# Kernel tuning notes

Hardware: AMD Instinct MI355X
Metric: run time of the kernel (lower is better)

The kernel has to match this reference:

```python
import jax, jax.numpy as jnp
import numpy as np


def _glorot(key, shape):
    lim = np.sqrt(6.0 / (shape[-2] + shape[-1])).astype(np.float32)
    return jax.random.uniform(key, shape, jnp.float32, -lim, lim)


def setup_inputs() -> dict:
    key = jax.random.key(0)
    B, F, K, L = 8192, 256, 32768, 4
    H = 2 * F          # CouplingLayer(feat_size, feat_size * 2) hidden width
    half = F // 2      # affine coupling transforms half the features
    ks = jax.random.split(key, 6)
    return {
        "inputs": jax.random.normal(ks[0], (B, F), jnp.float32),
        "W1": _glorot(ks[1], (L, half, H)),
        "b1": jnp.zeros((L, H), jnp.float32),
        "Ws": _glorot(ks[2], (L, H, half)),
        "bs": jnp.zeros((L, half), jnp.float32),
        "Wt": _glorot(ks[3], (L, H, half)),
        "bt": jnp.zeros((L, half), jnp.float32),
        "prior": _glorot(ks[4], (K, F)),  # VQ codebook, GlorotUniform init as in source
    }


def _forward_flow(x, W1, b1, Ws, bs, Wt, bt):
    """Stack of affine coupling layers; returns (y, log|det J|) per sample."""
    L = W1.shape[0]
    jac = jnp.zeros((x.shape[0],), x.dtype)
    for l in range(L):  # small fixed layer count
        xa, xb = jnp.split(x, 2, axis=1)                 # [B, F/2] each
        h = jax.nn.relu(xa @ W1[l] + b1[l])              # [B, 2F]
        s_raw = h @ Ws[l] + bs[l]                        # [B, F/2]
        s = s_raw if l == L - 1 else jnp.tanh(s_raw)     # last layer: tf.identity
        t = h @ Wt[l] + bt[l]
        yb = xb * jnp.exp(s) + t
        jac = jac + jnp.sum(s, axis=1)
        x = jnp.concatenate([yb, xa], axis=1)            # swap halves for mixing
    return x, jac


def reference(inputs, W1, b1, Ws, bs, Wt, bt, prior):
    sg = jax.lax.stop_gradient
    x, jac = _forward_flow(inputs, W1, b1, Ws, bs, Wt, bt)   # [B, F], [B]
    # pairwise squared distance to codebook: [B, K]
    na = jnp.sum(x * x, axis=1, keepdims=True)               # [B, 1]
    nb = jnp.sum(prior * prior, axis=1)[None, :]             # [1, K]
    d = jnp.maximum(na - 2.0 * (x @ prior.T) + nb, 0.0)      # [B, K]
    target_ind = jnp.argmin(d, axis=1)                       # [B]
    target = prior[target_ind]                               # gather, [B, F]
    loss_1 = jnp.mean(jnp.sum((x - sg(target)) ** 2, axis=1) / 2)
    loss_2 = jnp.mean(jnp.sum((sg(x) - target) ** 2, axis=1) / 2)
    loss = loss_1 + 0.25 * loss_2 - jnp.mean(jac)
    return x, loss
```

## Files before the change

### kernel.cpp

```cpp
#include <hip/hip_runtime.h>
#include <hip/hip_fp8.h>
#include <stdint.h>

#define NB     8192
#define NF     256
#define NHALF  128
#define NHID   512
#define NLAY   4
#define NK     32768

#define SX     (1.0f / 16.0f)
#define SP     (256.0f)

typedef __attribute__((ext_vector_type(8))) short bf16x8;
typedef __attribute__((ext_vector_type(4))) float f32x4;
typedef __attribute__((ext_vector_type(8))) int i32x8;

static __device__ __forceinline__ unsigned short f2bf(float f) {
  union { float f; unsigned int u; } v; v.f = f;
  return (unsigned short)((v.u + 0x7FFFu + ((v.u >> 16) & 1u)) >> 16);
}
static __device__ __forceinline__ float bf2f(unsigned short u) {
  union { unsigned int u; float f; } v; v.u = ((unsigned int)u) << 16; return v.f;
}
static __device__ __forceinline__ unsigned char f2fp8(float f) {
  __hip_fp8_e4m3 q(f);
  return (unsigned char)q.__x;
}
static __device__ __forceinline__ float fp82f(unsigned char b) {
  __hip_fp8_e4m3 q; q.__x = b; return (float)q;
}

static __device__ __forceinline__ void load_lds16(const void* g, void* l) {
  __builtin_amdgcn_global_load_lds(
      (const __attribute__((address_space(1))) unsigned int*)g,
      (__attribute__((address_space(3))) unsigned int*)l, 16, 0, 0);
}

static __device__ __forceinline__ unsigned long long packsi(float v, int idx) {
  unsigned int b = __float_as_uint(v);
  b = (b & 0x80000000u) ? ~b : (b | 0x80000000u);
  return ((unsigned long long)b << 32) | (unsigned int)(~(unsigned int)idx);
}

static __device__ __forceinline__ float fast_tanh(float x) {
  const float xc = fminf(fmaxf(x, -15.f), 15.f);
  const float e2 = __expf(2.f * xc);
  return 1.f - 2.f / (e2 + 1.f);
}

static __device__ __forceinline__ int swadr(int kseg, int nrows, int row, int kin) {
  return (kseg * nrows + row) * 64 + (((kin >> 3) ^ (row & 7)) * 8) + (kin & 7);
}

static __device__ __forceinline__ int g1swz(int row) {
  return (row & 15) ^ ((row & 8) >> 1);
}

static __device__ __forceinline__ void stage_chunk(
    int g, unsigned short* dst,
    const unsigned short* __restrict__ W1T,
    const unsigned short* __restrict__ W2I,
    int wave, int lane, int bxr)
{
  const int l = g >> 3;
  const int nc = ((g & 7) + bxr) & 7;
  const unsigned short* W1l = W1T + (size_t)l * (NHID * NHALF) + (size_t)nc * 64 * 128;
#pragma unroll
  for (int u = 0; u < 2; u++) {
    const int ch = (u * 8 + wave) * 64 + lane;
    const int row = ch >> 4, sl = ch & 15;
    load_lds16(W1l + (size_t)row * 128 + (sl ^ g1swz(row)) * 8, dst + ch * 8);
  }
  const unsigned short* W2l = W2I + (size_t)l * (NF * NHID) + nc * 64;
#pragma unroll
  for (int u = 0; u < 4; u++) {
    const int ch = (u * 8 + wave) * 64 + lane;
    const int col = ch >> 3, sl = ch & 7;
    load_lds16(W2l + (size_t)col * NHID + ((sl ^ (col & 7)) * 8),
               dst + 8192 + ch * 8);
  }
}

__global__ __launch_bounds__(512, 2)
void flow_all(const float* __restrict__ in,
              const unsigned short* __restrict__ W1T,
              const unsigned short* __restrict__ W2I,
              const float* __restrict__ b1A,
              const float* __restrict__ bsA,
              const float* __restrict__ btA,
              float* __restrict__ xout,
              unsigned char* __restrict__ xf8,
              float* __restrict__ jac)
{
  __shared__ __align__(16) unsigned short Xb[2][32 * 128];
  __shared__ __align__(16) unsigned short Bs[2][24576];
  __shared__ float b1s[NLAY * NHID];
  __shared__ float bss[NLAY * NHALF];
  __shared__ float bts[NLAY * NHALF];
  __shared__ float jlds[4][32];
  const int tid = threadIdx.x;
  const int lane = tid & 63, wave = tid >> 6;
  const int rg = wave >> 2, cg = wave & 3;
  const int q = lane >> 4, c = lane & 15;
  const int m0 = blockIdx.x * 32;
  const int bxr = blockIdx.x & 7;

  stage_chunk(0, Bs[0], W1T, W2I, wave, lane, bxr);

#pragma unroll
  for (int v = 0; v < 4; v++) {
    const int t4 = tid + v * 512;
    const int row = t4 >> 6, f4 = t4 & 63;
    const float4 d = *(const float4*)(in + (size_t)(m0 + row) * NF + f4 * 4);
    unsigned short* dst = Xb[f4 >> 5];
    const int feat = (f4 & 31) * 4;
    const float vals[4] = {d.x, d.y, d.z, d.w};
#pragma unroll
    for (int u = 0; u < 4; u++) {
      const int fe = feat + u;
      dst[swadr(fe >> 6, 32, row, fe & 63)] = f2bf(vals[u]);
    }
  }

#pragma unroll
  for (int v = 0; v < 4; v++) b1s[tid + v * 512] = b1A[tid + v * 512];
  bss[tid] = bsA[tid];
  bts[tid] = btA[tid];

  stage_chunk(1, Bs[1], W1T, W2I, wave, lane, bxr);

  float jr[4] = {0.f, 0.f, 0.f, 0.f};
  bf16x8 af1[4];
  const f32x4 z = {0.f, 0.f, 0.f, 0.f};
  f32x4 acc2[4];

  for (int g = 0; g < 32; g++) {
    if (g < 31)
      asm volatile("s_waitcnt vmcnt(6) lgkmcnt(0)\n\ts_barrier" ::: "memory");
    else
      asm volatile("s_waitcnt vmcnt(0) lgkmcnt(0)\n\ts_barrier" ::: "memory");

    const int l = g >> 3, s = g & 7;
    const int nc = (s + bxr) & 7;
    const unsigned short* B = Bs[g & 1];
    const unsigned short* W2B = B + 8192;
    unsigned short* XA = Xb[l & 1];
    unsigned short* XB = Xb[1 - (l & 1)];

    if (s == 0) {
#pragma unroll
      for (int kw = 0; kw < 4; kw++) {
        const int kch = kw * 4 + q;
        af1[kw] = *(const bf16x8*)(XA + ((kch >> 3) * 32 + rg * 16 + c) * 64 +
                                   (((kch & 7) ^ (c & 7)) * 8));
      }
#pragma unroll
      for (int j = 0; j < 4; j++) acc2[j] = z;
    }

    const int bias_base = l * NHID + nc * 64;
#pragma unroll
    for (int P = 0; P < 2; P++) {
      union { unsigned int u[4]; bf16x8 v; } a2;
#pragma unroll
      for (int tb = 0; tb < 2; tb++) {
        f32x4 acc1 = z;
        const int row = P * 32 + 8 * (c >> 2) + (c & 3) + 4 * tb;
        const int gsw = g1swz(row);
#pragma unroll
        for (int kk = 0; kk < 4; kk++) {
          const bf16x8 a1 = *(const bf16x8*)(B + row * 128 +
                                             (((kk * 4 + q) ^ gsw) * 8));
          acc1 = __builtin_amdgcn_mfma_f32_16x16x32_bf16(a1, af1[kk], acc1, 0, 0, 0);
        }
        const float4 bb = *(const float4*)(b1s + bias_base + P * 32 + 8 * q + 4 * tb);
        const float v0 = fmaxf(acc1[0] + bb.x, 0.f);
        const float v1 = fmaxf(acc1[1] + bb.y, 0.f);
        const float v2 = fmaxf(acc1[2] + bb.z, 0.f);
        const float v3 = fmaxf(acc1[3] + bb.w, 0.f);
        a2.u[tb * 2]     = (unsigned int)f2bf(v0) | ((unsigned int)f2bf(v1) << 16);
        a2.u[tb * 2 + 1] = (unsigned int)f2bf(v2) | ((unsigned int)f2bf(v3) << 16);
      }
#pragma unroll
      for (int j = 0; j < 4; j++) {
        const int col = cg * 64 + 16 * j + c;
        const bf16x8 b2 = *(const bf16x8*)(W2B + col * 64 +
                                           (((P * 4 + q) ^ (col & 7)) * 8));
        acc2[j] = __builtin_amdgcn_mfma_f32_16x16x32_bf16(a2.v, b2, acc2[j], 0, 0, 0);
      }
    }

    if (s == 7) {
      const int parity = c & 1;
      const int lastl = (l == NLAY - 1);
      const float* bsl = bss + l * NHALF;
      const float* btl = bts + l * NHALF;
#pragma unroll
      for (int j = 0; j < 4; j++) {
        const int col = cg * 64 + 16 * j + c;
#pragma unroll
        for (int r = 0; r < 4; r++) {
          const float val = acc2[j][r];
          const float oth = __shfl_xor(val, 1);
          if (!parity) {
            const int feat = col >> 1;
            float sv = val + bsl[feat];
            if (!lastl) sv = fast_tanh(sv);
            const float t = oth + btl[feat];
            const int row = rg * 16 + 4 * q + r;
            const int xaddr = swadr(feat >> 6, 32, row, feat & 63);
            const float xb = bf2f(XB[xaddr]);
            const float yb = xb * __expf(sv) + t;
            jr[r] += sv;
            XB[xaddr] = f2bf(yb);
            if (l >= 2) {
              const int k = lastl ? feat : (NHALF + feat);
              const size_t grow = (size_t)(m0 + row) * NF;
              xout[grow + k] = yb;
              xf8[(size_t)(m0 + row) * 256 + k] = f2fp8(yb * SX);
            }
          }
        }
      }
    }

    asm volatile("s_waitcnt lgkmcnt(0)\n\ts_barrier" ::: "memory");
    if (g + 2 < 32) stage_chunk(g + 2, Bs[g & 1], W1T, W2I, wave, lane, bxr);
  }

#pragma unroll
  for (int r = 0; r < 4; r++) {
    float v = jr[r];
    v += __shfl_xor(v, 1); v += __shfl_xor(v, 2);
    v += __shfl_xor(v, 4); v += __shfl_xor(v, 8);
    if (c == 0) jlds[cg][rg * 16 + 4 * q + r] = v;
  }
  __syncthreads();
  if (tid < 32)
    jac[m0 + tid] = jlds[0][tid] + jlds[1][tid] + jlds[2][tid] + jlds[3][tid];
}

__global__ __launch_bounds__(256, 2)
void vq_argmax(const unsigned char* __restrict__ X8,
               const unsigned char* __restrict__ P8,
               const float* __restrict__ nbh,
               unsigned long long* __restrict__ gbest)
{
  __shared__ __align__(16) unsigned char Bs[2][64 * 256];
  const int tid = threadIdx.x;
  const int lane = tid & 63, wave = tid >> 6;
  const int y = blockIdx.x & 15;
  const int m0 = (blockIdx.x >> 4) * 256;
  const int q = lane >> 4, c = lane & 15;
  const int mw = m0 + wave * 64;
  const int one = 0x7F7F7F7F;

  i32x8 af[4][2];
#pragma unroll
  for (int i = 0; i < 4; i++) {
    const unsigned char* xr = X8 + (size_t)(mw + 16 * i + c) * 256 + q * 32;
#pragma unroll
    for (int h = 0; h < 2; h++) {
      const int4 lo = *(const int4*)(xr + h * 128);
      const int4 hi = *(const int4*)(xr + h * 128 + 16);
      af[i][h] = (i32x8){lo.x, lo.y, lo.z, lo.w, hi.x, hi.y, hi.z, hi.w};
    }
  }

  float bestv[16];
  int besti[16];
#pragma unroll
  for (int t = 0; t < 16; t++) { bestv[t] = -1e30f; besti[t] = 0; }

  {
    const int n0s = y * 2048;
#pragma unroll
    for (int u = 0; u < 4; u++) {
      const int chb = (u * 4 + wave) * 64;
      const int ch = chb + lane;
      const int row = ch >> 4, gslot = ch & 15;
      load_lds16(P8 + (size_t)(n0s + row) * 256 + (gslot ^ (row & 15)) * 16,
                 Bs[0] + chb * 16);
    }
  }

  for (int nt = 0; nt < 32; nt++) {
    const int n0 = y * 2048 + nt * 64;
    __syncthreads();

    float nbr[4];
#pragma unroll
    for (int j = 0; j < 4; j++) nbr[j] = nbh[n0 + 16 * j + c];

    if (nt + 1 < 32) {
      const int n0s = n0 + 64;
      unsigned char* dst = Bs[(nt + 1) & 1];
#pragma unroll
      for (int u = 0; u < 4; u++) {
        const int chb = (u * 4 + wave) * 64;
        const int ch = chb + lane;
        const int row = ch >> 4, gslot = ch & 15;
        load_lds16(P8 + (size_t)(n0s + row) * 256 + (gslot ^ (row & 15)) * 16,
                   dst + chb * 16);
      }
    }

    const unsigned char* Bt = Bs[nt & 1];
    f32x4 acc[4][4];
#pragma unroll
    for (int i = 0; i < 4; i++)
#pragma unroll
      for (int j = 0; j < 4; j++)
        acc[i][j] = (f32x4){-nbr[j], -nbr[j], -nbr[j], -nbr[j]};

#pragma unroll
    for (int j = 0; j < 4; j++) {
      const unsigned char* base = Bt + (16 * j + c) * 256;
#pragma unroll
      for (int h = 0; h < 2; h++) {
        const int4 b0 = *(const int4*)(base + ((8 * h + 2 * q)     ^ c) * 16);
        const int4 b1 = *(const int4*)(base + ((8 * h + 2 * q + 1) ^ c) * 16);
        const i32x8 bf = (i32x8){b0.x, b0.y, b0.z, b0.w, b1.x, b1.y, b1.z, b1.w};
#pragma unroll
        for (int i = 0; i < 4; i++)
          acc[i][j] = __builtin_amdgcn_mfma_scale_f32_16x16x128_f8f6f4(
              af[i][h], bf, acc[i][j], 0, 0, 0, one, 0, one);
      }
    }

#pragma unroll
    for (int j = 0; j < 4; j++) {
      const int col = n0 + 16 * j + c;
#pragma unroll
      for (int i = 0; i < 4; i++)
#pragma unroll
        for (int r = 0; r < 4; r++) {
          const float sc = acc[i][j][r];
          const int t = i * 4 + r;
          if (sc > bestv[t]) { bestv[t] = sc; besti[t] = col; }
        }
    }
  }

#pragma unroll
  for (int t = 0; t < 16; t++) {
    float lv = bestv[t]; int li = besti[t];
#pragma unroll
    for (int mk = 8; mk >= 1; mk >>= 1) {
      const float ov = __shfl_xor(lv, mk);
      const int oi = __shfl_xor(li, mk);
      if (ov > lv || (ov == lv && oi < li)) { lv = ov; li = oi; }
    }
    if (c == 0) {
      const int row = mw + 16 * (t >> 2) + q * 4 + (t & 3);
      atomicMax(&gbest[row], packsi(lv, li));
    }
  }
}

__global__ void prep_all(const float* __restrict__ W1,
                         const float* __restrict__ Ws,
                         const float* __restrict__ Wt,
                         const float* __restrict__ prior,
                         unsigned short* __restrict__ W1T,
                         unsigned short* __restrict__ W2I,
                         unsigned char* __restrict__ p8,
                         float* __restrict__ nbh,
                         unsigned long long* __restrict__ gbest,
                         float* __restrict__ accum)
{
  __shared__ float ts[64 * 65];
  const int bx = blockIdx.x;
  const int tid = threadIdx.x;
  if (bx < 2048) {
    const int k = bx * 16 + (tid >> 4);
    const int l16 = tid & 15;
    float s = 0.f;
#pragma unroll
    for (int v = 0; v < 4; v++) {
      const int off = (v * 16 + l16) * 4;
      const float4 d = *(const float4*)(prior + (size_t)k * NF + off);
      uchar4 o;
      o.x = f2fp8(d.x * SP); o.y = f2fp8(d.y * SP);
      o.z = f2fp8(d.z * SP); o.w = f2fp8(d.w * SP);
      *(uchar4*)(p8 + (size_t)k * 256 + off) = o;
      const float q0 = fp82f(o.x), q1 = fp82f(o.y), q2 = fp82f(o.z), q3 = fp82f(o.w);
      s += q0 * q0 + q1 * q1 + q2 * q2 + q3 * q3;
    }
#pragma unroll
    for (int mk = 8; mk >= 1; mk >>= 1) s += __shfl_xor(s, mk);
    if (l16 == 0) nbh[k] = 0.5f * s * (SX / SP);
  } else if (bx < 2112) {
    const int job = bx - 2048;
    const int l = job >> 4, t = job & 15;
    const int k0 = (t >> 3) * 64, n0 = (t & 7) * 64;
    const float* src = W1 + (size_t)l * NHALF * NHID;
#pragma unroll
    for (int v = 0; v < 16; v++) {
      const int e = tid + v * 256;
      const int kk = e >> 6, nn = e & 63;
      ts[kk * 65 + nn] = src[(size_t)(k0 + kk) * NHID + n0 + nn];
    }
    __syncthreads();
    unsigned short* dst = W1T + (size_t)l * NHID * NHALF;
#pragma unroll
    for (int v = 0; v < 16; v++) {
      const int e = tid + v * 256;
      const int nn = e >> 6, kk = e & 63;
      dst[(size_t)(n0 + nn) * NHALF + k0 + kk] = f2bf(ts[kk * 65 + nn]);
    }
  } else if (bx < 2240) {
    const int job = bx - 2112;
    const int l = job >> 5, rem = job & 31;
    const int b = rem >> 4;
    const int k0 = ((rem >> 1) & 7) * 64;
    const int f0 = (rem & 1) * 64;
    const float* src = (b ? Wt : Ws) + (size_t)l * NHID * NHALF;
#pragma unroll
    for (int v = 0; v < 16; v++) {
      const int e = tid + v * 256;
      const int kk = e >> 6, nn = e & 63;
      ts[kk * 65 + nn] = src[(size_t)(k0 + kk) * NHALF + f0 + nn];
    }
    __syncthreads();
#pragma unroll
    for (int v = 0; v < 16; v++) {
      const int e = tid + v * 256;
      const int nn = e >> 6, kk = e & 63;
      W2I[((size_t)l * NF + 2 * (f0 + nn) + b) * NHID + k0 + kk] = f2bf(ts[kk * 65 + nn]);
    }
  } else {
    const int idx = (bx - 2240) * 256 + tid;
    if (idx < NB) gbest[idx] = 0ull;
    if (idx < 4) accum[idx] = 0.f;
  }
}

__global__ void vq_finalize(const float* __restrict__ X,
                            const float* __restrict__ prior,
                            const unsigned long long* __restrict__ gbest,
                            const float* __restrict__ jac,
                            float* __restrict__ accum,
                            float* __restrict__ loss)
{
  const int wave = threadIdx.x >> 6, lane = threadIdx.x & 63;
  const int gw = blockIdx.x * 4 + wave;
  float accd = 0.f, accj = 0.f;
  for (int r = 0; r < 8; r++) {
    const int row = gw * 8 + r;
    const unsigned int idx = ~(unsigned int)(gbest[row]);
    const float* x = X + (size_t)row * NF;
    const float* p = prior + (size_t)idx * NF;
#pragma unroll
    for (int u = 0; u < 4; u++) {
      const int d = lane + u * 64;
      const float df = x[d] - p[d];
      accd += df * df;
    }
    if (lane == 0) accj += jac[row];
  }
#pragma unroll
  for (int mk = 32; mk >= 1; mk >>= 1) {
    accd += __shfl_xor(accd, mk);
    accj += __shfl_xor(accj, mk);
  }
  __shared__ float sd[4], sj[4];
  if (lane == 0) { sd[wave] = accd; sj[wave] = accj; }
  __syncthreads();
  if (threadIdx.x == 0) {
    atomicAdd(&accum[0], sd[0] + sd[1] + sd[2] + sd[3]);
    atomicAdd(&accum[1], sj[0] + sj[1] + sj[2] + sj[3]);
    __threadfence();
    const unsigned int t = atomicAdd((unsigned int*)&accum[2], 1u);
    if (t == 255u) {
      const float d = atomicAdd(&accum[0], 0.f);
      const float jv = atomicAdd(&accum[1], 0.f);
      loss[0] = 1.25f * (0.5f * d / (float)NB) - jv / (float)NB;
    }
  }
}

extern "C" void kernel_launch(void* const* d_in, const int* in_sizes, int n_in,
                              void* d_out, int out_size, void* d_ws, size_t ws_size,
                              hipStream_t stream)
{
  (void)in_sizes; (void)n_in; (void)out_size; (void)ws_size;
  const float* inputs = (const float*)d_in[0];
  const float* W1 = (const float*)d_in[1];
  const float* b1 = (const float*)d_in[2];
  const float* Ws = (const float*)d_in[3];
  const float* bs = (const float*)d_in[4];
  const float* Wt = (const float*)d_in[5];
  const float* bt = (const float*)d_in[6];
  const float* prior = (const float*)d_in[7];

  char* p = (char*)d_ws;
  auto alloc = [&](size_t bytes) { char* r = p; p += (bytes + 255) & ~(size_t)255; return r; };
  unsigned short* W1T  = (unsigned short*)alloc((size_t)NLAY * NHID * NHALF * 2);
  unsigned short* W2I  = (unsigned short*)alloc((size_t)NLAY * NF * NHID * 2);
  unsigned char* P8    = (unsigned char*)alloc((size_t)NK * 256);
  float* NBH           = (float*)alloc((size_t)NK * 4);
  unsigned char* XF8   = (unsigned char*)alloc((size_t)NB * 256);
  float* JAC           = (float*)alloc((size_t)NB * 4);
  unsigned long long* GBEST = (unsigned long long*)alloc((size_t)NB * 8);
  float* ACC           = (float*)alloc(256);

  float* xout = (float*)d_out;
  float* loss = xout + (size_t)NB * NF;

  prep_all<<<dim3(2272), 256, 0, stream>>>(
      W1, Ws, Wt, prior, W1T, W2I, P8, NBH, GBEST, ACC);

  flow_all<<<dim3(NB / 32), 512, 0, stream>>>(
      inputs, W1T, W2I, b1, bs, bt, xout, XF8, JAC);

  vq_argmax<<<dim3(32 * 16), 256, 0, stream>>>(XF8, P8, NBH, GBEST);
  vq_finalize<<<dim3(256), 256, 0, stream>>>(xout, prior, GBEST, JAC, ACC, loss);
}
```

Baseline: 237.4 us.

## Fuse codebook fp8 quantization into flow kernel and finalize into argmax kernel

Measured after the change: 305.4 us. 28.6% more time.

```diff
diff --git a/kernel.cpp b/kernel.cpp
--- a/kernel.cpp
+++ b/kernel.cpp
@@ -16,6 +16,15 @@
 typedef __attribute__((ext_vector_type(4))) float f32x4;
 typedef __attribute__((ext_vector_type(8))) int i32x8;
 
+#if defined(__has_builtin)
+#  if __has_builtin(__builtin_amdgcn_cvt_pk_fp8_f32)
+#    define HAVE_HW_FP8_ENC 1
+#  endif
+#  if __has_builtin(__builtin_amdgcn_cvt_f32_fp8)
+#    define HAVE_HW_FP8_DEC 1
+#  endif
+#endif
+
 static __device__ __forceinline__ unsigned short f2bf(float f) {
   union { float f; unsigned int u; } v; v.f = f;
   return (unsigned short)((v.u + 0x7FFFu + ((v.u >> 16) & 1u)) >> 16);
@@ -23,12 +32,34 @@
 static __device__ __forceinline__ float bf2f(unsigned short u) {
   union { unsigned int u; float f; } v; v.u = ((unsigned int)u) << 16; return v.f;
 }
-static __device__ __forceinline__ unsigned char f2fp8(float f) {
+static __device__ __forceinline__ unsigned char f2fp8_sw(float f) {
   __hip_fp8_e4m3 q(f);
   return (unsigned char)q.__x;
 }
-static __device__ __forceinline__ float fp82f(unsigned char b) {
-  __hip_fp8_e4m3 q; q.__x = b; return (float)q;
+static __device__ __forceinline__ unsigned char f2fp8(float f) {
+#ifdef HAVE_HW_FP8_ENC
+  return (unsigned char)(__builtin_amdgcn_cvt_pk_fp8_f32(f, f, 0, false) & 0xff);
+#else
+  return f2fp8_sw(f);
+#endif
+}
+static __device__ __forceinline__ unsigned int fp8x4(float a, float b, float c, float d) {
+#ifdef HAVE_HW_FP8_ENC
+  int v = __builtin_amdgcn_cvt_pk_fp8_f32(a, b, 0, false);
+  v = __builtin_amdgcn_cvt_pk_fp8_f32(c, d, v, true);
+  return (unsigned int)v;
+#else
+  return (unsigned int)f2fp8_sw(a) | ((unsigned int)f2fp8_sw(b) << 8) |
+         ((unsigned int)f2fp8_sw(c) << 16) | ((unsigned int)f2fp8_sw(d) << 24);
+#endif
+}
+template <int SEL>
+static __device__ __forceinline__ float fp8dec(unsigned int w) {
+#ifdef HAVE_HW_FP8_DEC
+  return __builtin_amdgcn_cvt_f32_fp8((int)w, SEL);
+#else
+  __hip_fp8_e4m3 q; q.__x = (unsigned char)(w >> (8 * SEL)); return (float)q;
+#endif
 }
 
 static __device__ __forceinline__ void load_lds16(const void* g, void* l) {
@@ -82,15 +113,18 @@
   }
 }
 
-__global__ __launch_bounds__(512, 2)
+__global__ __launch_bounds__(768, 1)
 void flow_all(const float* __restrict__ in,
               const unsigned short* __restrict__ W1T,
               const unsigned short* __restrict__ W2I,
               const float* __restrict__ b1A,
               const float* __restrict__ bsA,
               const float* __restrict__ btA,
+              const float* __restrict__ prior,
               float* __restrict__ xout,
               unsigned char* __restrict__ xf8,
+              unsigned char* __restrict__ p8,
+              float* __restrict__ nbh,
               float* __restrict__ jac)
 {
   __shared__ __align__(16) unsigned short Xb[2][32 * 128];
@@ -101,34 +135,35 @@
   __shared__ float jlds[4][32];
   const int tid = threadIdx.x;
   const int lane = tid & 63, wave = tid >> 6;
-  const int rg = wave >> 2, cg = wave & 3;
+  const int rg = (wave >> 2) & 1, cg = wave & 3;
   const int q = lane >> 4, c = lane & 15;
   const int m0 = blockIdx.x * 32;
   const int bxr = blockIdx.x & 7;
 
-  stage_chunk(0, Bs[0], W1T, W2I, wave, lane, bxr);
-
-#pragma unroll
-  for (int v = 0; v < 4; v++) {
-    const int t4 = tid + v * 512;
-    const int row = t4 >> 6, f4 = t4 & 63;
-    const float4 d = *(const float4*)(in + (size_t)(m0 + row) * NF + f4 * 4);
-    unsigned short* dst = Xb[f4 >> 5];
-    const int feat = (f4 & 31) * 4;
-    const float vals[4] = {d.x, d.y, d.z, d.w};
-#pragma unroll
-    for (int u = 0; u < 4; u++) {
-      const int fe = feat + u;
-      dst[swadr(fe >> 6, 32, row, fe & 63)] = f2bf(vals[u]);
-    }
-  }
-
-#pragma unroll
-  for (int v = 0; v < 4; v++) b1s[tid + v * 512] = b1A[tid + v * 512];
-  bss[tid] = bsA[tid];
-  bts[tid] = btA[tid];
-
-  stage_chunk(1, Bs[1], W1T, W2I, wave, lane, bxr);
+  if (wave < 8) stage_chunk(0, Bs[0], W1T, W2I, wave, lane, bxr);
+
+  if (tid < 512) {
+#pragma unroll
+    for (int v = 0; v < 4; v++) {
+      const int t4 = tid + v * 512;
+      const int row = t4 >> 6, f4 = t4 & 63;
+      const float4 d = *(const float4*)(in + (size_t)(m0 + row) * NF + f4 * 4);
+      unsigned short* dst = Xb[f4 >> 5];
+      const int feat = (f4 & 31) * 4;
+      const float vals[4] = {d.x, d.y, d.z, d.w};
+#pragma unroll
+      for (int u = 0; u < 4; u++) {
+        const int fe = feat + u;
+        dst[swadr(fe >> 6, 32, row, fe & 63)] = f2bf(vals[u]);
+      }
+    }
+#pragma unroll
+    for (int v = 0; v < 4; v++) b1s[tid + v * 512] = b1A[tid + v * 512];
+    bss[tid] = bsA[tid];
+    bts[tid] = btA[tid];
+  }
+
+  if (wave < 8) stage_chunk(1, Bs[1], W1T, W2I, wave, lane, bxr);
 
   float jr[4] = {0.f, 0.f, 0.f, 0.f};
   bf16x8 af1[4];
@@ -136,105 +171,122 @@
   f32x4 acc2[4];
 
   for (int g = 0; g < 32; g++) {
-    if (g < 31)
-      asm volatile("s_waitcnt vmcnt(6) lgkmcnt(0)\n\ts_barrier" ::: "memory");
-    else
-      asm volatile("s_waitcnt vmcnt(0) lgkmcnt(0)\n\ts_barrier" ::: "memory");
-
-    const int l = g >> 3, s = g & 7;
-    const int nc = (s + bxr) & 7;
-    const unsigned short* B = Bs[g & 1];
-    const unsigned short* W2B = B + 8192;
-    unsigned short* XA = Xb[l & 1];
-    unsigned short* XB = Xb[1 - (l & 1)];
-
-    if (s == 0) {
-#pragma unroll
-      for (int kw = 0; kw < 4; kw++) {
-        const int kch = kw * 4 + q;
-        af1[kw] = *(const bf16x8*)(XA + ((kch >> 3) * 32 + rg * 16 + c) * 64 +
-                                   (((kch & 7) ^ (c & 7)) * 8));
-      }
-#pragma unroll
-      for (int j = 0; j < 4; j++) acc2[j] = z;
-    }
-
-    const int bias_base = l * NHID + nc * 64;
-#pragma unroll
-    for (int P = 0; P < 2; P++) {
-      union { unsigned int u[4]; bf16x8 v; } a2;
-#pragma unroll
-      for (int tb = 0; tb < 2; tb++) {
-        f32x4 acc1 = z;
-        const int row = P * 32 + 8 * (c >> 2) + (c & 3) + 4 * tb;
-        const int gsw = g1swz(row);
-#pragma unroll
-        for (int kk = 0; kk < 4; kk++) {
-          const bf16x8 a1 = *(const bf16x8*)(B + row * 128 +
-                                             (((kk * 4 + q) ^ gsw) * 8));
-          acc1 = __builtin_amdgcn_mfma_f32_16x16x32_bf16(a1, af1[kk], acc1, 0, 0, 0);
+    if (wave < 8) {
+      if (g < 31)
+        asm volatile("s_waitcnt vmcnt(6) lgkmcnt(0)\n\ts_barrier" ::: "memory");
+      else
+        asm volatile("s_waitcnt vmcnt(0) lgkmcnt(0)\n\ts_barrier" ::: "memory");
+
+      const int l = g >> 3, s = g & 7;
+      const int nc = (s + bxr) & 7;
+      const unsigned short* B = Bs[g & 1];
+      const unsigned short* W2B = B + 8192;
+      unsigned short* XA = Xb[l & 1];
+      unsigned short* XB = Xb[1 - (l & 1)];
+
+      if (s == 0) {
+#pragma unroll
+        for (int kw = 0; kw < 4; kw++) {
+          const int kch = kw * 4 + q;
+          af1[kw] = *(const bf16x8*)(XA + ((kch >> 3) * 32 + rg * 16 + c) * 64 +
+                                     (((kch & 7) ^ (c & 7)) * 8));
         }
-        const float4 bb = *(const float4*)(b1s + bias_base + P * 32 + 8 * q + 4 * tb);
-        const float v0 = fmaxf(acc1[0] + bb.x, 0.f);
-        const float v1 = fmaxf(acc1[1] + bb.y, 0.f);
-        const float v2 = fmaxf(acc1[2] + bb.z, 0.f);
-        const float v3 = fmaxf(acc1[3] + bb.w, 0.f);
-        a2.u[tb * 2]     = (unsigned int)f2bf(v0) | ((unsigned int)f2bf(v1) << 16);
-        a2.u[tb * 2 + 1] = (unsigned int)f2bf(v2) | ((unsigned int)f2bf(v3) << 16);
-      }
-#pragma unroll
-      for (int j = 0; j < 4; j++) {
-        const int col = cg * 64 + 16 * j + c;
-        const bf16x8 b2 = *(const bf16x8*)(W2B + col * 64 +
-                                           (((P * 4 + q) ^ (col & 7)) * 8));
-        acc2[j] = __builtin_amdgcn_mfma_f32_16x16x32_bf16(a2.v, b2, acc2[j], 0, 0, 0);
-      }
-    }
-
-    if (s == 7) {
-      const int parity = c & 1;
-      const int lastl = (l == NLAY - 1);
-      const float* bsl = bss + l * NHALF;
-      const float* btl = bts + l * NHALF;
-#pragma unroll
-      for (int j = 0; j < 4; j++) {
-        const int col = cg * 64 + 16 * j + c;
-#pragma unroll
-        for (int r = 0; r < 4; r++) {
-          const float val = acc2[j][r];
-          const float oth = __shfl_xor(val, 1);
-          if (!parity) {
-            const int feat = col >> 1;
-            float sv = val + bsl[feat];
-            if (!lastl) sv = fast_tanh(sv);
-            const float t = oth + btl[feat];
-            const int row = rg * 16 + 4 * q + r;
-            const int xaddr = swadr(feat >> 6, 32, row, feat & 63);
-            const float xb = bf2f(XB[xaddr]);
-            const float yb = xb * __expf(sv) + t;
-            jr[r] += sv;
-            XB[xaddr] = f2bf(yb);
-            if (l >= 2) {
-              const int k = lastl ? feat : (NHALF + feat);
-              const size_t grow = (size_t)(m0 + row) * NF;
-              xout[grow + k] = yb;
-              xf8[(size_t)(m0 + row) * 256 + k] = f2fp8(yb * SX);
+#pragma unroll
+        for (int j = 0; j < 4; j++) acc2[j] = z;
+      }
+
+      const int bias_base = l * NHID + nc * 64;
+#pragma unroll
+      for (int P = 0; P < 2; P++) {
+        union { unsigned int u[4]; bf16x8 v; } a2;
+#pragma unroll
+        for (int tb = 0; tb < 2; tb++) {
+          f32x4 acc1 = z;
+          const int row = P * 32 + 8 * (c >> 2) + (c & 3) + 4 * tb;
+          const int gsw = g1swz(row);
+#pragma unroll
+          for (int kk = 0; kk < 4; kk++) {
+            const bf16x8 a1 = *(const bf16x8*)(B + row * 128 +
+                                               (((kk * 4 + q) ^ gsw) * 8));
+            acc1 = __builtin_amdgcn_mfma_f32_16x16x32_bf16(a1, af1[kk], acc1, 0, 0, 0);
+          }
+          const float4 bb = *(const float4*)(b1s + bias_base + P * 32 + 8 * q + 4 * tb);
+          const float v0 = fmaxf(acc1[0] + bb.x, 0.f);
+          const float v1 = fmaxf(acc1[1] + bb.y, 0.f);
+          const float v2 = fmaxf(acc1[2] + bb.z, 0.f);
+          const float v3 = fmaxf(acc1[3] + bb.w, 0.f);
+          a2.u[tb * 2]     = (unsigned int)f2bf(v0) | ((unsigned int)f2bf(v1) << 16);
+          a2.u[tb * 2 + 1] = (unsigned int)f2bf(v2) | ((unsigned int)f2bf(v3) << 16);
+        }
+#pragma unroll
+        for (int j = 0; j < 4; j++) {
+          const int col = cg * 64 + 16 * j + c;
+          const bf16x8 b2 = *(const bf16x8*)(W2B + col * 64 +
+                                             (((P * 4 + q) ^ (col & 7)) * 8));
+          acc2[j] = __builtin_amdgcn_mfma_f32_16x16x32_bf16(a2.v, b2, acc2[j], 0, 0, 0);
+        }
+      }
+
+      if (s == 7) {
+        const int parity = c & 1;
+        const int lastl = (l == NLAY - 1);
+        const float* bsl = bss + l * NHALF;
+        const float* btl = bts + l * NHALF;
+#pragma unroll
+        for (int j = 0; j < 4; j++) {
+          const int col = cg * 64 + 16 * j + c;
+#pragma unroll
+          for (int r = 0; r < 4; r++) {
+            const float val = acc2[j][r];
+            const float oth = __shfl_xor(val, 1);
+            if (!parity) {
+              const int feat = col >> 1;
+              float sv = val + bsl[feat];
+              if (!lastl) sv = fast_tanh(sv);
+              const float t = oth + btl[feat];
+              const int row = rg * 16 + 4 * q + r;
+              const int xaddr = swadr(feat >> 6, 32, row, feat & 63);
+              const float xb = bf2f(XB[xaddr]);
+              const float yb = xb * __expf(sv) + t;
+              jr[r] += sv;
+              XB[xaddr] = f2bf(yb);
+              if (l >= 2) {
+                const int k = lastl ? feat : (NHALF + feat);
+                const size_t grow = (size_t)(m0 + row) * NF;
+                xout[grow + k] = yb;
+                xf8[(size_t)(m0 + row) * 256 + k] = f2fp8(yb * SX);
+              }
             }
           }
         }
       }
-    }
-
-    asm volatile("s_waitcnt lgkmcnt(0)\n\ts_barrier" ::: "memory");
-    if (g + 2 < 32) stage_chunk(g + 2, Bs[g & 1], W1T, W2I, wave, lane, bxr);
-  }
-
-#pragma unroll
-  for (int r = 0; r < 4; r++) {
-    float v = jr[r];
-    v += __shfl_xor(v, 1); v += __shfl_xor(v, 2);
-    v += __shfl_xor(v, 4); v += __shfl_xor(v, 8);
-    if (c == 0) jlds[cg][rg * 16 + 4 * q + r] = v;
+
+      asm volatile("s_waitcnt lgkmcnt(0)\n\ts_barrier" ::: "memory");
+      if (g + 2 < 32) stage_chunk(g + 2, Bs[g & 1], W1T, W2I, wave, lane, bxr);
+    } else {
+      const int code = (((int)blockIdx.x * 4 + (wave - 8)) << 5) + g;
+      const float4 d = *(const float4*)(prior + (size_t)code * NF + lane * 4);
+      const unsigned int w4 = fp8x4(d.x * SP, d.y * SP, d.z * SP, d.w * SP);
+      *(unsigned int*)(p8 + (size_t)code * 256 + lane * 4) = w4;
+      const float q0 = fp8dec<0>(w4), q1 = fp8dec<1>(w4);
+      const float q2 = fp8dec<2>(w4), q3 = fp8dec<3>(w4);
+      float s = q0 * q0 + q1 * q1 + q2 * q2 + q3 * q3;
+#pragma unroll
+      for (int mk = 32; mk >= 1; mk >>= 1) s += __shfl_xor(s, mk);
+      if (lane == 0) nbh[code] = 0.5f * s * (SX / SP);
+      asm volatile("s_barrier" ::: "memory");
+      asm volatile("s_barrier" ::: "memory");
+    }
+  }
+
+  if (wave < 8) {
+#pragma unroll
+    for (int r = 0; r < 4; r++) {
+      float v = jr[r];
+      v += __shfl_xor(v, 1); v += __shfl_xor(v, 2);
+      v += __shfl_xor(v, 4); v += __shfl_xor(v, 8);
+      if (c == 0) jlds[cg][rg * 16 + 4 * q + r] = v;
+    }
   }
   __syncthreads();
   if (tid < 32)
@@ -245,13 +297,20 @@
 void vq_argmax(const unsigned char* __restrict__ X8,
                const unsigned char* __restrict__ P8,
                const float* __restrict__ nbh,
-               unsigned long long* __restrict__ gbest)
+               unsigned long long* __restrict__ gbest,
+               const float* __restrict__ X,
+               const float* __restrict__ priorF,
+               const float* __restrict__ jac,
+               float* __restrict__ accum,
+               unsigned int* __restrict__ tick,
+               float* __restrict__ loss)
 {
   __shared__ __align__(16) unsigned char Bs[2][64 * 256];
   const int tid = threadIdx.x;
   const int lane = tid & 63, wave = tid >> 6;
   const int y = blockIdx.x & 15;
-  const int m0 = (blockIdx.x >> 4) * 256;
+  const int mgrp = blockIdx.x >> 4;
+  const int m0 = mgrp * 256;
   const int q = lane >> 4, c = lane & 15;
   const int mw = m0 + wave * 64;
   const int one = 0x7F7F7F7F;
@@ -357,42 +416,65 @@
       atomicMax(&gbest[row], packsi(lv, li));
     }
   }
-}
-
-__global__ void prep_all(const float* __restrict__ W1,
-                         const float* __restrict__ Ws,
-                         const float* __restrict__ Wt,
-                         const float* __restrict__ prior,
-                         unsigned short* __restrict__ W1T,
-                         unsigned short* __restrict__ W2I,
-                         unsigned char* __restrict__ p8,
-                         float* __restrict__ nbh,
-                         unsigned long long* __restrict__ gbest,
-                         float* __restrict__ accum)
+
+  __threadfence();
+  __shared__ int lastf;
+  if (tid == 0) lastf = (atomicAdd(&tick[mgrp], 1u) == 15u);
+  __syncthreads();
+  if (lastf) {
+    __threadfence();
+    float accd = 0.f, accj = 0.f;
+    for (int r = 0; r < 64; r++) {
+      const int row = m0 + wave * 64 + r;
+      unsigned long long gv = 0ull;
+      if (lane == 0) gv = atomicMax(&gbest[row], 0ull);
+      gv = __shfl(gv, 0);
+      const unsigned int idx = ~(unsigned int)gv;
+      const float* xr = X + (size_t)row * NF;
+      const float* pr = priorF + (size_t)idx * NF;
+#pragma unroll
+      for (int u = 0; u < 4; u++) {
+        const int dd = lane + u * 64;
+        const float df = xr[dd] - pr[dd];
+        accd += df * df;
+      }
+      if (lane == 0) accj += jac[row];
+    }
+#pragma unroll
+    for (int mk = 32; mk >= 1; mk >>= 1) {
+      accd += __shfl_xor(accd, mk);
+      accj += __shfl_xor(accj, mk);
+    }
+    __shared__ float sd[4], sj[4];
+    if (lane == 0) { sd[wave] = accd; sj[wave] = accj; }
+    __syncthreads();
+    if (tid == 0) {
+      atomicAdd(&accum[0], sd[0] + sd[1] + sd[2] + sd[3]);
+      atomicAdd(&accum[1], sj[0] + sj[1] + sj[2] + sj[3]);
+      __threadfence();
+      const unsigned int t2 = atomicAdd((unsigned int*)&accum[2], 1u);
+      if (t2 == 31u) {
+        const float dsum = atomicAdd(&accum[0], 0.f);
+        const float jsum = atomicAdd(&accum[1], 0.f);
+        loss[0] = 1.25f * (0.5f * dsum / (float)NB) - jsum / (float)NB;
+      }
+    }
+  }
+}
+
+__global__ void prep_W(const float* __restrict__ W1,
+                       const float* __restrict__ Ws,
+                       const float* __restrict__ Wt,
+                       unsigned short* __restrict__ W1T,
+                       unsigned short* __restrict__ W2I,
+                       unsigned long long* __restrict__ gbest,
+                       float* __restrict__ accum)
 {
   __shared__ float ts[64 * 65];
   const int bx = blockIdx.x;
   const int tid = threadIdx.x;
-  if (bx < 2048) {
-    const int k = bx * 16 + (tid >> 4);
-    const int l16 = tid & 15;
-    float s = 0.f;
-#pragma unroll
-    for (int v = 0; v < 4; v++) {
-      const int off = (v * 16 + l16) * 4;
-      const float4 d = *(const float4*)(prior + (size_t)k * NF + off);
-      uchar4 o;
-      o.x = f2fp8(d.x * SP); o.y = f2fp8(d.y * SP);
-      o.z = f2fp8(d.z * SP); o.w = f2fp8(d.w * SP);
-      *(uchar4*)(p8 + (size_t)k * 256 + off) = o;
-      const float q0 = fp82f(o.x), q1 = fp82f(o.y), q2 = fp82f(o.z), q3 = fp82f(o.w);
-      s += q0 * q0 + q1 * q1 + q2 * q2 + q3 * q3;
-    }
-#pragma unroll
-    for (int mk = 8; mk >= 1; mk >>= 1) s += __shfl_xor(s, mk);
-    if (l16 == 0) nbh[k] = 0.5f * s * (SX / SP);
-  } else if (bx < 2112) {
-    const int job = bx - 2048;
+  if (bx < 64) {
+    const int job = bx;
     const int l = job >> 4, t = job & 15;
     const int k0 = (t >> 3) * 64, n0 = (t & 7) * 64;
     const float* src = W1 + (size_t)l * NHALF * NHID;
@@ -410,8 +492,8 @@
       const int nn = e >> 6, kk = e & 63;
       dst[(size_t)(n0 + nn) * NHALF + k0 + kk] = f2bf(ts[kk * 65 + nn]);
     }
-  } else if (bx < 2240) {
-    const int job = bx - 2112;
+  } else if (bx < 192) {
+    const int job = bx - 64;
     const int l = job >> 5, rem = job & 31;
     const int b = rem >> 4;
     const int k0 = ((rem >> 1) & 7) * 64;
@@ -431,53 +513,9 @@
       W2I[((size_t)l * NF + 2 * (f0 + nn) + b) * NHID + k0 + kk] = f2bf(ts[kk * 65 + nn]);
     }
   } else {
-    const int idx = (bx - 2240) * 256 + tid;
+    const int idx = (bx - 192) * 256 + tid;
     if (idx < NB) gbest[idx] = 0ull;
-    if (idx < 4) accum[idx] = 0.f;
-  }
-}
-
-__global__ void vq_finalize(const float* __restrict__ X,
-                            const float* __restrict__ prior,
-                            const unsigned long long* __restrict__ gbest,
-                            const float* __restrict__ jac,
-                            float* __restrict__ accum,
-                            float* __restrict__ loss)
-{
-  const int wave = threadIdx.x >> 6, lane = threadIdx.x & 63;
-  const int gw = blockIdx.x * 4 + wave;
-  float accd = 0.f, accj = 0.f;
-  for (int r = 0; r < 8; r++) {
-    const int row = gw * 8 + r;
-    const unsigned int idx = ~(unsigned int)(gbest[row]);
-    const float* x = X + (size_t)row * NF;
-    const float* p = prior + (size_t)idx * NF;
-#pragma unroll
-    for (int u = 0; u < 4; u++) {
-      const int d = lane + u * 64;
-      const float df = x[d] - p[d];
-      accd += df * df;
-    }
-    if (lane == 0) accj += jac[row];
-  }
-#pragma unroll
-  for (int mk = 32; mk >= 1; mk >>= 1) {
-    accd += __shfl_xor(accd, mk);
-    accj += __shfl_xor(accj, mk);
-  }
-  __shared__ float sd[4], sj[4];
-  if (lane == 0) { sd[wave] = accd; sj[wave] = accj; }
-  __syncthreads();
-  if (threadIdx.x == 0) {
-    atomicAdd(&accum[0], sd[0] + sd[1] + sd[2] + sd[3]);
-    atomicAdd(&accum[1], sj[0] + sj[1] + sj[2] + sj[3]);
-    __threadfence();
-    const unsigned int t = atomicAdd((unsigned int*)&accum[2], 1u);
-    if (t == 255u) {
-      const float d = atomicAdd(&accum[0], 0.f);
-      const float jv = atomicAdd(&accum[1], 0.f);
-      loss[0] = 1.25f * (0.5f * d / (float)NB) - jv / (float)NB;
-    }
+    if (idx < 64) accum[idx] = 0.f;
   }
 }
 
@@ -505,16 +543,16 @@
   float* JAC           = (float*)alloc((size_t)NB * 4);
   unsigned long long* GBEST = (unsigned long long*)alloc((size_t)NB * 8);
   float* ACC           = (float*)alloc(256);
+  unsigned int* TICK   = (unsigned int*)(ACC + 8);
 
   float* xout = (float*)d_out;
   float* loss = xout + (size_t)NB * NF;
 
-  prep_all<<<dim3(2272), 256, 0, stream>>>(
-      W1, Ws, Wt, prior, W1T, W2I, P8, NBH, GBEST, ACC);
-
-  flow_all<<<dim3(NB / 32), 512, 0, stream>>>(
-      inputs, W1T, W2I, b1, bs, bt, xout, XF8, JAC);
-
-  vq_argmax<<<dim3(32 * 16), 256, 0, stream>>>(XF8, P8, NBH, GBEST);
-  vq_finalize<<<dim3(256), 256, 0, stream>>>(xout, prior, GBEST, JAC, ACC, loss);
-}
+  prep_W<<<dim3(224), 256, 0, stream>>>(W1, Ws, Wt, W1T, W2I, GBEST, ACC);
+
+  flow_all<<<dim3(NB / 32), 768, 0, stream>>>(
+      inputs, W1T, W2I, b1, bs, bt, prior, xout, XF8, P8, NBH, JAC);
+
+  vq_argmax<<<dim3(32 * 16), 256, 0, stream>>>(
+      XF8, P8, NBH, GBEST, xout, prior, JAC, ACC, TICK, loss);
+}
```
